# Kernel optimization log

Hardware: AMD Instinct MI355X
Metric: run time of the kernel (lower is better)

The kernel has to match this reference:

```python
import jax, jax.numpy as jnp
import numpy as np


def setup_inputs() -> dict:
    key = jax.random.key(0)
    k1, k2 = jax.random.split(key)
    B, D, T = 16, 256, 1500
    N_Q, BINS = 8, 1024
    x = jax.random.normal(k1, (B, D, T), dtype=jnp.float32)
    codebooks = jax.random.normal(k2, (N_Q, BINS, D), dtype=jnp.float32)
    return {"x": x, "codebooks": codebooks, "n_q": N_Q}


def reference(x, codebooks, n_q):
    """Residual VQ forward (EnCodec-style).

    x: (B, D, T) float32; codebooks: (n_q_total, bins, D); n_q: python int.
    Returns (quantized (B,D,T), codes (n_q,B,T) int32, penalty scalar).
    """
    B, D, T = x.shape
    residual = jnp.transpose(x, (0, 2, 1)).reshape(B * T, D)  # (N, D)
    quant_out = jnp.zeros_like(residual)
    codes = []
    losses = []
    for q in range(n_q):
        cb = codebooks[q]                      # (K, D)
        # nearest neighbor under L2: argmin ||r-c||^2 == argmax 2 r.c - ||c||^2
        dots = residual @ cb.T                 # (N, K) GEMM
        cb_sq = jnp.sum(cb * cb, axis=1)       # (K,)
        idx = jnp.argmax(2.0 * dots - cb_sq, axis=1)  # (N,)
        quant = cb[idx]                        # gather (N, D)
        # commitment loss: mse(quantize.detach(), layer input)
        losses.append(jnp.mean((jax.lax.stop_gradient(quant) - residual) ** 2))
        # straight-through estimator
        quant_st = residual + jax.lax.stop_gradient(quant - residual)
        residual = residual - quant_st
        quant_out = quant_out + quant_st
        codes.append(idx.astype(jnp.int32))
    quantized = jnp.transpose(quant_out.reshape(B, T, D), (0, 2, 1))  # (B, D, T)
    codes = jnp.stack(codes, axis=0).reshape(n_q, B, T)
    penalty = jnp.mean(jnp.stack(losses))
    return quantized, codes, penalty
```

## Files before the change

kernel.cpp:

```cpp
#include <hip/hip_runtime.h>
#include <math.h>

#define NBATCH 16
#define DDIM   256
#define TLEN   1500
#define NROWS  (NBATCH * TLEN)
#define KBINS  1024
#define NQ     8
#define RPB    32
#define QMAX   1024

typedef float  f32x4  __attribute__((ext_vector_type(4)));
typedef short  short8 __attribute__((ext_vector_type(8)));
union Frag { uint4 u; short8 s; };

__device__ __forceinline__ unsigned cvtpk(float a, float b) {
    unsigned r;
    asm("v_cvt_pk_bf16_f32 %0, %1, %2" : "=v"(r) : "v"(a), "v"(b));
    return r;
}

__device__ __forceinline__ void barrier_lds() {
    __builtin_amdgcn_sched_barrier(0);
    asm volatile("s_waitcnt lgkmcnt(0)" ::: "memory");
    __builtin_amdgcn_s_barrier();
    __builtin_amdgcn_sched_barrier(0);
}

__global__ __launch_bounds__(256) void cbsq_kernel(const float* __restrict__ cb,
                                                   float* __restrict__ ws) {
    const int k = blockIdx.x * 256 + threadIdx.x;
    if (blockIdx.x == 0 && threadIdx.x < NQ) ws[NQ * KBINS + threadIdx.x] = 0.f;
    if (k >= NQ * KBINS) return;
    const float* p = cb + (size_t)k * DDIM;
    float total = 0.f;
    #pragma unroll
    for (int h = 0; h < 2; ++h) {
        const float* ph = p + h * 128;
        float r[8];
        #pragma unroll
        for (int j = 0; j < 8; ++j) { float v = ph[j]; r[j] = __fmul_rn(v, v); }
        for (int i = 8; i < 128; i += 8) {
            #pragma unroll
            for (int j = 0; j < 8; ++j) {
                float v = ph[i + j];
                r[j] = __fadd_rn(r[j], __fmul_rn(v, v));
            }
        }
        float s = __fadd_rn(__fadd_rn(__fadd_rn(r[0], r[1]), __fadd_rn(r[2], r[3])),
                            __fadd_rn(__fadd_rn(r[4], r[5]), __fadd_rn(r[6], r[7])));
        total = __fadd_rn(total, s);
    }
    ws[k] = total;
}

__global__ __launch_bounds__(256) void precvt_kernel(const float* __restrict__ cb,
                                                     unsigned* __restrict__ cbbf) {
    const int j = blockIdx.x * 256 + threadIdx.x;
    const int e  = j & 3;
    const int l  = (j >> 2) & 63;
    const int ks = (j >> 8) & 7;
    const int w  = (j >> 11) & 3;
    const int ch = (j >> 13) & 15;
    const int q  = j >> 17;
    const int C  = ch * 64 + w * 16 + (l & 15);
    const int g  = l >> 4;
    const int s  = ks * 16 + g * 2 + ((e >> 1) << 3) + (e & 1);
    const float* src = cb + ((size_t)q * KBINS + C) * DDIM + 2 * s;
    cbbf[j] = cvtpk(src[0], src[1]);
}

template<bool WSCB>
__global__ __launch_bounds__(256, 2) void rvq_kernel(const float* __restrict__ x,
                                                     const float* __restrict__ cb,
                                                     const unsigned* __restrict__ cbbf,
                                                     const float* __restrict__ cbsq_g,
                                                     float* __restrict__ loss,
                                                     float* __restrict__ out) {
    __shared__ __align__(16) float As[RPB][260];
    __shared__ float cbsqs[KBINS];
    __shared__ float rsq[RPB];
    __shared__ float Mrow_s[RPB];
    __shared__ float Mpart[2][4][RPB];
    __shared__ unsigned long long winner[RPB];
    __shared__ int   idxs[RPB];
    __shared__ int   qlist[QMAX];
    __shared__ int   qcnt;
    __shared__ float redpart[4];
    __shared__ float cmaxs;

    const int tid = threadIdx.x;
    const int r0  = blockIdx.x * RPB;
    const int w   = tid >> 6;
    const int l   = tid & 63;
    const int cl  = l & 15;
    const int g   = l >> 4;

    const uint4* cbbf4 = (const uint4*)cbbf;

    if (tid < RPB) rsq[tid] = 0.f;
    barrier_lds();

    {
        const int row = tid & 31, dg = tid >> 5;
        const int n = r0 + row, b = n / TLEN, t = n % TLEN;
        const float* xp = x + (size_t)b * (DDIM * TLEN) + t;
        float pr = 0.f;
        #pragma unroll
        for (int dd = 0; dd < DDIM; dd += 8) {
            float v = xp[(size_t)(dd + dg) * TLEN];
            As[row][dd + dg] = v;
            pr = __builtin_fmaf(v, v, pr);
        }
        atomicAdd(&rsq[row], pr);
    }
    barrier_lds();

    float* codes_f = out + (size_t)NBATCH * DDIM * TLEN;

    auto loadB = [&](uint4 (&buf)[8], int q_, int ch_) {
        if constexpr (WSCB) {
            const uint4* p = cbbf4 + ((size_t)((q_ * 16 + ch_) * 4 + w) * 8) * 64 + l;
            #pragma unroll
            for (int ks = 0; ks < 8; ++ks) buf[ks] = p[ks * 64];
        } else {
            const float* cp = cb + ((size_t)q_ * KBINS + ch_ * 64 + w * 16 + cl) * DDIM;
            #pragma unroll
            for (int ks = 0; ks < 8; ++ks) {
                const int d0 = ks * 32 + g * 4;
                float4 v0 = *(const float4*)(cp + d0);
                float4 v1 = *(const float4*)(cp + d0 + 16);
                buf[ks].x = cvtpk(v0.x, v0.y);
                buf[ks].y = cvtpk(v0.z, v0.w);
                buf[ks].z = cvtpk(v1.x, v1.y);
                buf[ks].w = cvtpk(v1.z, v1.w);
            }
        }
    };

    uint4 bufA[8], bufB[8];
    loadB(bufA, 0, 0);
    __builtin_amdgcn_sched_barrier(0);

    for (int q = 0; q < NQ; ++q) {
        const float* cbq = cb + (size_t)q * (KBINS * DDIM);

        float c4m = -INFINITY;
        #pragma unroll
        for (int j = 0; j < 4; ++j) {
            float v = cbsq_g[q * KBINS + tid + j * 256];
            cbsqs[tid + j * 256] = v;
            c4m = fmaxf(c4m, v);
        }
        #pragma unroll
        for (int m = 1; m < 64; m <<= 1) c4m = fmaxf(c4m, __shfl_xor(c4m, m, 64));
        if (l == 0) redpart[w] = c4m;

        Frag af[2][8];
        #pragma unroll
        for (int mt = 0; mt < 2; ++mt)
            #pragma unroll
            for (int ks = 0; ks < 8; ++ks) {
                const float* ap = &As[mt * 16 + cl][ks * 32 + 4 * g];
                float4 x0 = *(const float4*)ap;
                float4 x1 = *(const float4*)(ap + 16);
                af[mt][ks].u.x = cvtpk(x0.x, x0.y);
                af[mt][ks].u.y = cvtpk(x0.z, x0.w);
                af[mt][ks].u.z = cvtpk(x1.x, x1.y);
                af[mt][ks].u.w = cvtpk(x1.z, x1.w);
            }

        if (tid < RPB) { Mrow_s[tid] = -INFINITY; winner[tid] = 0ull; }
        if (tid == 0) qcnt = 0;
        barrier_lds();
        if (tid == 0)
            cmaxs = sqrtf(fmaxf(fmaxf(redpart[0], redpart[1]),
                                fmaxf(redpart[2], redpart[3])));

        for (int quarter = 0; quarter < 4; ++quarter) {
            const int par = quarter & 1;
            float m_lane[2][4];
            #pragma unroll
            for (int mt = 0; mt < 2; ++mt)
                #pragma unroll
                for (int r = 0; r < 4; ++r) m_lane[mt][r] = -INFINITY;
            unsigned spack[4][2][2];

            #pragma unroll
            for (int cc = 0; cc < 4; ++cc) {
                const int ch = quarter * 4 + cc;
                uint4 (&cur)[8] = (cc & 1) ? bufB : bufA;
                uint4 (&nxt)[8] = (cc & 1) ? bufA : bufB;

                int pq = q, pch = ch + 1;
                if (ch == 15) { pq = (q < NQ - 1) ? q + 1 : q; pch = 0; }
                loadB(nxt, pq, pch);
                __builtin_amdgcn_sched_barrier(0);

                f32x4 aE0, aO0, aE1, aO1;
                #pragma unroll
                for (int r = 0; r < 4; ++r) { aE0[r] = 0.f; aO0[r] = 0.f; aE1[r] = 0.f; aO1[r] = 0.f; }
                #pragma unroll
                for (int ks = 0; ks < 8; ks += 2) {
                    Frag b0; b0.u = cur[ks];
                    Frag b1; b1.u = cur[ks + 1];
                    aE0 = __builtin_amdgcn_mfma_f32_16x16x32_bf16(af[0][ks].s,     b0.s, aE0, 0, 0, 0);
                    aE1 = __builtin_amdgcn_mfma_f32_16x16x32_bf16(af[1][ks].s,     b0.s, aE1, 0, 0, 0);
                    aO0 = __builtin_amdgcn_mfma_f32_16x16x32_bf16(af[0][ks + 1].s, b1.s, aO0, 0, 0, 0);
                    aO1 = __builtin_amdgcn_mfma_f32_16x16x32_bf16(af[1][ks + 1].s, b1.s, aO1, 0, 0, 0);
                }

                const float sqv = cbsqs[ch * 64 + w * 16 + cl];
                {
                    float s0 = 2.f * (aE0[0] + aO0[0]) - sqv, s1 = 2.f * (aE0[1] + aO0[1]) - sqv;
                    float s2 = 2.f * (aE0[2] + aO0[2]) - sqv, s3 = 2.f * (aE0[3] + aO0[3]) - sqv;
                    m_lane[0][0] = fmaxf(m_lane[0][0], s0);
                    m_lane[0][1] = fmaxf(m_lane[0][1], s1);
                    m_lane[0][2] = fmaxf(m_lane[0][2], s2);
                    m_lane[0][3] = fmaxf(m_lane[0][3], s3);
                    spack[cc][0][0] = (__float_as_uint(s1) & 0xFFFF0000u) | (__float_as_uint(s0) >> 16);
                    spack[cc][0][1] = (__float_as_uint(s3) & 0xFFFF0000u) | (__float_as_uint(s2) >> 16);
                }
                {
                    float s0 = 2.f * (aE1[0] + aO1[0]) - sqv, s1 = 2.f * (aE1[1] + aO1[1]) - sqv;
                    float s2 = 2.f * (aE1[2] + aO1[2]) - sqv, s3 = 2.f * (aE1[3] + aO1[3]) - sqv;
                    m_lane[1][0] = fmaxf(m_lane[1][0], s0);
                    m_lane[1][1] = fmaxf(m_lane[1][1], s1);
                    m_lane[1][2] = fmaxf(m_lane[1][2], s2);
                    m_lane[1][3] = fmaxf(m_lane[1][3], s3);
                    spack[cc][1][0] = (__float_as_uint(s1) & 0xFFFF0000u) | (__float_as_uint(s0) >> 16);
                    spack[cc][1][1] = (__float_as_uint(s3) & 0xFFFF0000u) | (__float_as_uint(s2) >> 16);
                }
            }

            #pragma unroll
            for (int m = 1; m <= 8; m <<= 1)
                #pragma unroll
                for (int mt = 0; mt < 2; ++mt)
                    #pragma unroll
                    for (int r = 0; r < 4; ++r)
                        m_lane[mt][r] = fmaxf(m_lane[mt][r], __shfl_xor(m_lane[mt][r], m, 64));
            if (cl == 0) {
                #pragma unroll
                for (int mt = 0; mt < 2; ++mt)
                    #pragma unroll
                    for (int r = 0; r < 4; ++r)
                        Mpart[par][w][mt * 16 + g * 4 + r] = m_lane[mt][r];
            }
            barrier_lds();

            float thrl[2][4];
            #pragma unroll
            for (int mt = 0; mt < 2; ++mt)
                #pragma unroll
                for (int jj = 0; jj < 4; ++jj) {
                    const int r = mt * 16 + g * 4 + jj;
                    float M = fmaxf(fmaxf(Mpart[par][0][r], Mpart[par][1][r]),
                                    fmaxf(Mpart[par][2][r], Mpart[par][3][r]));
                    float Mr = fmaxf(Mrow_s[r], M);
                    Mrow_s[r] = Mr;
                    float margin = 0.02f * sqrtf(rsq[r]) * cmaxs
                                 + 0.006f * fabsf(Mr) + 0.25f;
                    thrl[mt][jj] = Mr - margin;
                }

            #pragma unroll
            for (int cc = 0; cc < 4; ++cc) {
                const int colc = (quarter * 4 + cc) * 64 + w * 16 + cl;
                #pragma unroll
                for (int mt = 0; mt < 2; ++mt)
                    #pragma unroll
                    for (int pr = 0; pr < 2; ++pr) {
                        unsigned u = spack[cc][mt][pr];
                        float slo = __uint_as_float(u << 16);
                        float shi = __uint_as_float(u & 0xFFFF0000u);
                        if (slo >= thrl[mt][pr * 2]) {
                            int p = atomicAdd(&qcnt, 1);
                            if (p < QMAX) qlist[p] = ((mt * 16 + g * 4 + pr * 2) << 10) | colc;
                        }
                        if (shi >= thrl[mt][pr * 2 + 1]) {
                            int p = atomicAdd(&qcnt, 1);
                            if (p < QMAX) qlist[p] = ((mt * 16 + g * 4 + pr * 2 + 1) << 10) | colc;
                        }
                    }
            }
        }
        barrier_lds();

        {
            int nc = qcnt < QMAX ? qcnt : QMAX;
            for (int i = tid; i < nc; i += 256) {
                const int rc = qlist[i];
                const int row = rc >> 10, col = rc & 1023;
                const float* cp = cbq + (size_t)col * DDIM;
                float dot = 0.f;
                #pragma unroll 8
                for (int d = 0; d < DDIM; d += 4) {
                    float4 c4 = *(const float4*)(cp + d);
                    const float* ar = &As[row][d];
                    dot = __builtin_fmaf(ar[0], c4.x, dot);
                    dot = __builtin_fmaf(ar[1], c4.y, dot);
                    dot = __builtin_fmaf(ar[2], c4.z, dot);
                    dot = __builtin_fmaf(ar[3], c4.w, dot);
                }
                float sx = __fsub_rn(__fmul_rn(2.f, dot), cbsqs[col]);
                unsigned ub = __float_as_uint(sx);
                ub = (ub & 0x80000000u) ? ~ub : (ub | 0x80000000u);
                unsigned long long key = ((unsigned long long)ub << 10) | (unsigned)(1023 - col);
                atomicMax(&winner[row], key);
            }
        }
        barrier_lds();
        if (tid < RPB) {
            int col = 1023 - (int)(winner[tid] & 1023ull);
            idxs[tid] = col;
            codes_f[(size_t)q * NROWS + r0 + tid] = (float)col;
            rsq[tid] = 0.f;
        }
        barrier_lds();

        {
            const int row = tid & 31, d0 = (tid >> 5) * 32;
            const float* crow = cbq + (size_t)idxs[row] * DDIM + d0;
            float lp = 0.f, pr = 0.f;
            #pragma unroll
            for (int u = 0; u < 32; u += 4) {
                const float4 c4 = *(const float4*)(crow + u);
                const float cv[4] = { c4.x, c4.y, c4.z, c4.w };
                #pragma unroll
                for (int v = 0; v < 4; ++v) {
                    const float r   = As[row][d0 + u + v];
                    const float tmp = __fsub_rn(cv[v], r);
                    const float qs  = __fadd_rn(r, tmp);
                    const float rn  = __fsub_rn(r, qs);
                    As[row][d0 + u + v] = rn;
                    lp = __builtin_fmaf(tmp, tmp, lp);
                    pr = __builtin_fmaf(rn, rn, pr);
                }
            }
            #pragma unroll
            for (int m = 1; m < 64; m <<= 1) lp += __shfl_xor(lp, m, 64);
            if (l == 0) atomicAdd(&loss[q], lp);
            atomicAdd(&rsq[row], pr);
        }
        barrier_lds();
    }

    {
        const int row = tid & 31, dg = tid >> 5;
        const int n = r0 + row, b = n / TLEN, t = n % TLEN;
        const float* xp = x + (size_t)b * (DDIM * TLEN) + t;
        float* op = out + (size_t)b * (DDIM * TLEN) + t;
        #pragma unroll
        for (int u = 0; u < 32; ++u) {
            const int d = dg * 32 + u;
            op[(size_t)d * TLEN] = __fsub_rn(xp[(size_t)d * TLEN], As[row][d]);
        }
    }
}

__global__ void finalize_kernel(const float* __restrict__ loss, float* __restrict__ out) {
    if (threadIdx.x == 0 && blockIdx.x == 0) {
        float s = 0.f;
        for (int q = 0; q < NQ; ++q) s += loss[q] / (float)(NROWS * DDIM);
        out[(size_t)NBATCH * DDIM * TLEN + (size_t)NQ * NROWS] = s / (float)NQ;
    }
}

extern "C" void kernel_launch(void* const* d_in, const int* in_sizes, int n_in,
                              void* d_out, int out_size, void* d_ws, size_t ws_size,
                              hipStream_t stream) {
    const float* x  = (const float*)d_in[0];
    const float* cb = (const float*)d_in[1];
    float* out  = (float*)d_out;
    float* ws   = (float*)d_ws;
    float* cbsq = ws;
    float* loss = ws + NQ * KBINS;
    unsigned* cbbf = (unsigned*)(ws + 8224);
    const bool wsbf = ws_size >= (size_t)(8224 + (size_t)NQ * KBINS * DDIM / 2) * 4;

    hipLaunchKernelGGL(cbsq_kernel, dim3((NQ * KBINS) / 256), dim3(256), 0, stream, cb, ws);
    if (wsbf) {
        hipLaunchKernelGGL(precvt_kernel, dim3((NQ * KBINS * DDIM / 2) / 256), dim3(256),
                           0, stream, cb, cbbf);
        hipLaunchKernelGGL((rvq_kernel<true>), dim3(NROWS / RPB), dim3(256), 0, stream,
                           x, cb, cbbf, cbsq, loss, out);
    } else {
        hipLaunchKernelGGL((rvq_kernel<false>), dim3(NROWS / RPB), dim3(256), 0, stream,
                           x, cb, cbbf, cbsq, loss, out);
    }
    hipLaunchKernelGGL(finalize_kernel, dim3(1), dim3(64), 0, stream, loss, out);
}
```

Measured before the change: 445.0 us.

## Shrink candidate list, raise occupancy, rescore overflow inline, vectorize LDS access

Cuts the LDS candidate list from 1024 to 384 entries and raises the launch-bounds minimum from 2 to 4 blocks per CU, so more waves can be resident and hide latency. When the list overflows, a candidate is now rescored exactly on the spot instead of being dropped, which keeps the result correct under the smaller buffer. The exact rescoring and the residual update now read and write shared memory as float4 vectors, and the per-block cmax value is computed by every thread instead of being broadcast through shared memory. Forcing 4 blocks per CU may cause register spills in the MFMA-heavy loop, and the inline overflow path adds divergence.

```diff
diff --git a/kernel.cpp b/kernel.cpp
--- a/kernel.cpp
+++ b/kernel.cpp
@@ -8,7 +8,7 @@
 #define KBINS  1024
 #define NQ     8
 #define RPB    32
-#define QMAX   1024
+#define QMAX   384
 
 typedef float  f32x4  __attribute__((ext_vector_type(4)));
 typedef short  short8 __attribute__((ext_vector_type(8)));
@@ -71,7 +71,7 @@
 }
 
 template<bool WSCB>
-__global__ __launch_bounds__(256, 2) void rvq_kernel(const float* __restrict__ x,
+__global__ __launch_bounds__(256, 4) void rvq_kernel(const float* __restrict__ x,
                                                      const float* __restrict__ cb,
                                                      const unsigned* __restrict__ cbbf,
                                                      const float* __restrict__ cbsq_g,
@@ -87,7 +87,6 @@
     __shared__ int   qlist[QMAX];
     __shared__ int   qcnt;
     __shared__ float redpart[4];
-    __shared__ float cmaxs;
 
     const int tid = threadIdx.x;
     const int r0  = blockIdx.x * RPB;
@@ -145,6 +144,26 @@
     for (int q = 0; q < NQ; ++q) {
         const float* cbq = cb + (size_t)q * (KBINS * DDIM);
 
+        auto exact_score = [&](int row, int col) {
+            const float* cp = cbq + (size_t)col * DDIM;
+            const float* ar = As[row];
+            float dot = 0.f;
+            #pragma unroll 16
+            for (int d = 0; d < DDIM; d += 4) {
+                float4 c4 = *(const float4*)(cp + d);
+                float4 a4 = *(const float4*)(ar + d);
+                dot = __builtin_fmaf(a4.x, c4.x, dot);
+                dot = __builtin_fmaf(a4.y, c4.y, dot);
+                dot = __builtin_fmaf(a4.z, c4.z, dot);
+                dot = __builtin_fmaf(a4.w, c4.w, dot);
+            }
+            float sx = __fsub_rn(__fmul_rn(2.f, dot), cbsqs[col]);
+            unsigned ub = __float_as_uint(sx);
+            ub = (ub & 0x80000000u) ? ~ub : (ub | 0x80000000u);
+            unsigned long long key = ((unsigned long long)ub << 10) | (unsigned)(1023 - col);
+            atomicMax(&winner[row], key);
+        };
+
         float c4m = -INFINITY;
         #pragma unroll
         for (int j = 0; j < 4; ++j) {
@@ -173,9 +192,9 @@
         if (tid < RPB) { Mrow_s[tid] = -INFINITY; winner[tid] = 0ull; }
         if (tid == 0) qcnt = 0;
         barrier_lds();
-        if (tid == 0)
-            cmaxs = sqrtf(fmaxf(fmaxf(redpart[0], redpart[1]),
-                                fmaxf(redpart[2], redpart[3])));
+
+        const float cmax = sqrtf(fmaxf(fmaxf(redpart[0], redpart[1]),
+                                       fmaxf(redpart[2], redpart[3])));
 
         for (int quarter = 0; quarter < 4; ++quarter) {
             const int par = quarter & 1;
@@ -259,7 +278,7 @@
                                     fmaxf(Mpart[par][2][r], Mpart[par][3][r]));
                     float Mr = fmaxf(Mrow_s[r], M);
                     Mrow_s[r] = Mr;
-                    float margin = 0.02f * sqrtf(rsq[r]) * cmaxs
+                    float margin = 0.02f * sqrtf(rsq[r]) * cmax
                                  + 0.006f * fabsf(Mr) + 0.25f;
                     thrl[mt][jj] = Mr - margin;
                 }
@@ -275,12 +294,16 @@
                         float slo = __uint_as_float(u << 16);
                         float shi = __uint_as_float(u & 0xFFFF0000u);
                         if (slo >= thrl[mt][pr * 2]) {
+                            const int row = mt * 16 + g * 4 + pr * 2;
                             int p = atomicAdd(&qcnt, 1);
-                            if (p < QMAX) qlist[p] = ((mt * 16 + g * 4 + pr * 2) << 10) | colc;
+                            if (__builtin_expect(p < QMAX, 1)) qlist[p] = (row << 10) | colc;
+                            else exact_score(row, colc);
                         }
                         if (shi >= thrl[mt][pr * 2 + 1]) {
+                            const int row = mt * 16 + g * 4 + pr * 2 + 1;
                             int p = atomicAdd(&qcnt, 1);
-                            if (p < QMAX) qlist[p] = ((mt * 16 + g * 4 + pr * 2 + 1) << 10) | colc;
+                            if (__builtin_expect(p < QMAX, 1)) qlist[p] = (row << 10) | colc;
+                            else exact_score(row, colc);
                         }
                     }
             }
@@ -291,23 +314,7 @@
             int nc = qcnt < QMAX ? qcnt : QMAX;
             for (int i = tid; i < nc; i += 256) {
                 const int rc = qlist[i];
-                const int row = rc >> 10, col = rc & 1023;
-                const float* cp = cbq + (size_t)col * DDIM;
-                float dot = 0.f;
-                #pragma unroll 8
-                for (int d = 0; d < DDIM; d += 4) {
-                    float4 c4 = *(const float4*)(cp + d);
-                    const float* ar = &As[row][d];
-                    dot = __builtin_fmaf(ar[0], c4.x, dot);
-                    dot = __builtin_fmaf(ar[1], c4.y, dot);
-                    dot = __builtin_fmaf(ar[2], c4.z, dot);
-                    dot = __builtin_fmaf(ar[3], c4.w, dot);
-                }
-                float sx = __fsub_rn(__fmul_rn(2.f, dot), cbsqs[col]);
-                unsigned ub = __float_as_uint(sx);
-                ub = (ub & 0x80000000u) ? ~ub : (ub | 0x80000000u);
-                unsigned long long key = ((unsigned long long)ub << 10) | (unsigned)(1023 - col);
-                atomicMax(&winner[row], key);
+                exact_score(rc >> 10, rc & 1023);
             }
         }
         barrier_lds();
@@ -322,21 +329,25 @@
         {
             const int row = tid & 31, d0 = (tid >> 5) * 32;
             const float* crow = cbq + (size_t)idxs[row] * DDIM + d0;
+            float* arow = &As[row][d0];
             float lp = 0.f, pr = 0.f;
             #pragma unroll
             for (int u = 0; u < 32; u += 4) {
                 const float4 c4 = *(const float4*)(crow + u);
+                const float4 a4 = *(const float4*)(arow + u);
                 const float cv[4] = { c4.x, c4.y, c4.z, c4.w };
+                const float rv[4] = { a4.x, a4.y, a4.z, a4.w };
+                float rn[4];
                 #pragma unroll
                 for (int v = 0; v < 4; ++v) {
-                    const float r   = As[row][d0 + u + v];
-                    const float tmp = __fsub_rn(cv[v], r);
-                    const float qs  = __fadd_rn(r, tmp);
-                    const float rn  = __fsub_rn(r, qs);
-                    As[row][d0 + u + v] = rn;
+                    const float tmp = __fsub_rn(cv[v], rv[v]);
+                    const float qs  = __fadd_rn(rv[v], tmp);
+                    rn[v] = __fsub_rn(rv[v], qs);
                     lp = __builtin_fmaf(tmp, tmp, lp);
-                    pr = __builtin_fmaf(rn, rn, pr);
+                    pr = __builtin_fmaf(rn[v], rn[v], pr);
                 }
+                float4 o4; o4.x = rn[0]; o4.y = rn[1]; o4.z = rn[2]; o4.w = rn[3];
+                *(float4*)(arow + u) = o4;
             }
             #pragma unroll
             for (int m = 1; m < 64; m <<= 1) lp += __shfl_xor(lp, m, 64);
```

Result: slower. 1.142 ms (+156.7%).
